# Performance work log

Hardware: AMD Instinct MI355X
Metric: run time of the kernel (lower is better)

The kernel has to match this reference:

```python
import jax, jax.numpy as jnp
import numpy as np

B, N, F, C = 8, 256, 59, 128
BOX = 20.0
EPS = 1e-5


def _bn(y, g, b, m, v):
    # eval-mode BatchNorm1d over the channel (last) axis
    return (y - m) * jax.lax.rsqrt(v + EPS) * g + b


def setup_inputs() -> dict:
    key = jax.random.key(0)
    ks = jax.random.split(key, 12)
    x = jax.random.normal(ks[0], (B, N, F), jnp.float32)
    pos = jax.random.uniform(ks[1], (B, N, 3), jnp.float32) * BOX
    nrm = jax.random.normal(ks[2], (B, N, 3), jnp.float32)
    normal = nrm / jnp.linalg.norm(nrm, axis=-1, keepdims=True)
    s_in = 1.0 / np.sqrt(F)
    W_lin = jax.random.normal(ks[3], (C, F), jnp.float32) * s_in
    W_src = jax.random.normal(ks[4], (C, F), jnp.float32) * s_in
    W_dst = jax.random.normal(ks[5], (C, F), jnp.float32) * s_in
    pos_w = jax.random.normal(ks[6], (C, 6), jnp.float32) * (1.0 / np.sqrt(6.0))
    pos_b = jax.random.normal(ks[7], (C,), jnp.float32) * 0.02
    attn_w = jax.random.normal(ks[8], (C, C), jnp.float32) * (1.0 / np.sqrt(C))
    attn_b = jax.random.normal(ks[9], (C,), jnp.float32) * 0.02
    pos_bn_g = 1.0 + 0.1 * jax.random.normal(ks[10], (C,), jnp.float32)
    attn_bn_g = 1.0 + 0.1 * jax.random.normal(ks[11], (C,), jnp.float32)
    zeros = jnp.zeros((C,), jnp.float32)
    ones = jnp.ones((C,), jnp.float32)
    return {
        'x': x, 'pos': pos, 'normal': normal,
        'W_lin': W_lin, 'W_src': W_src, 'W_dst': W_dst,
        'pos_w': pos_w, 'pos_b': pos_b,
        'pos_bn_g': pos_bn_g, 'pos_bn_b': zeros, 'pos_bn_m': zeros, 'pos_bn_v': ones,
        'attn_w': attn_w, 'attn_b': attn_b,
        'attn_bn_g': attn_bn_g, 'attn_bn_b': zeros, 'attn_bn_m': zeros, 'attn_bn_v': ones,
        'r': 5,
    }


def reference(x, pos, normal, W_lin, W_src, W_dst, pos_w, pos_b,
              pos_bn_g, pos_bn_b, pos_bn_m, pos_bn_v,
              attn_w, attn_b, attn_bn_g, attn_bn_b, attn_bn_m, attn_bn_v, r):
    r = jnp.float32(r)
    # linear projections (bias-free, as in PyG PointTransformerConv)
    v = jnp.einsum('bnf,cf->bnc', x, W_lin)      # values
    a_src = jnp.einsum('bnf,cf->bnc', x, W_src)  # alpha for source j
    a_dst = jnp.einsum('bnf,cf->bnc', x, W_dst)  # alpha for dest   i
    # relative geometry, axis 1 = receiver i, axis 2 = sender j
    rel_pos = pos[:, :, None, :] - pos[:, None, :, :]          # [B,i,j,3]
    rel_nrm = normal[:, :, None, :] - normal[:, None, :, :]    # [B,i,j,3]
    relf = jnp.concatenate([rel_pos, rel_nrm], axis=-1)        # [B,i,j,6]
    # pos_nn = Linear(6,C) + BN + ReLU (eval)
    delta = jax.nn.relu(_bn(jnp.einsum('bijk,ck->bijc', relf, pos_w) + pos_b,
                            pos_bn_g, pos_bn_b, pos_bn_m, pos_bn_v))
    # attn_nn(alpha_i - alpha_j + delta)
    alpha_arg = a_dst[:, :, None, :] - a_src[:, None, :, :] + delta
    scores = jax.nn.relu(_bn(jnp.einsum('bijc,dc->bijd', alpha_arg, attn_w) + attn_b,
                             attn_bn_g, attn_bn_b, attn_bn_m, attn_bn_v))
    # radius mask within each graph (self-loops included, dist 0 <= r)
    dist2 = jnp.sum(rel_pos * rel_pos, axis=-1)                # [B,i,j]
    mask = (dist2 <= r * r)[..., None]                         # [B,i,j,1]
    attn = jax.nn.softmax(jnp.where(mask, scores, -jnp.inf), axis=2)
    # per-channel vector attention over neighbors j: sum_j attn * (v_j + delta)
    out = jnp.sum(attn * (v[:, None, :, :] + delta), axis=2)   # [B,i,C]
    return out
```

## Files before the change

kernel.cpp:

```cpp
#include <hip/hip_runtime.h>

typedef _Float16 h2 __attribute__((ext_vector_type(2)));
typedef _Float16 f16x8 __attribute__((ext_vector_type(8)));
typedef float f32x4 __attribute__((ext_vector_type(4)));
typedef unsigned int uint32;

#define BB 8
#define NN 256
#define FF 59
#define CC 128
#define EPSV 1e-5f

#define WS_V     0
#define WS_ASRC  (WS_V + BB*NN*CC)
#define WS_ADST  (WS_ASRC + BB*NN*CC)
#define WS_PWT   (WS_ADST + BB*NN*CC)
#define WS_T1    (WS_PWT + 6*CC)
#define WS_T2    (WS_T1 + CC)
#define WS_WTB   (WS_T2 + CC)

__global__ __launch_bounds__(256) void prep_kernel(
    const float* __restrict__ x, const float* __restrict__ W_lin,
    const float* __restrict__ W_src, const float* __restrict__ W_dst,
    const float* __restrict__ pos_w, const float* __restrict__ pos_b,
    const float* __restrict__ pos_g, const float* __restrict__ pos_bb,
    const float* __restrict__ pos_m, const float* __restrict__ pos_v,
    const float* __restrict__ attn_w, const float* __restrict__ attn_b,
    const float* __restrict__ attn_g, const float* __restrict__ attn_bb,
    const float* __restrict__ attn_m, const float* __restrict__ attn_v,
    float* __restrict__ ws)
{
    int blk = blockIdx.x;
    int tid = threadIdx.x;
    if (blk < 768) {
        int type = blk >> 8;
        int g    = blk & 255;
        int b    = g >> 5;
        int n0   = (g & 31) * 8;
        const float* W = (type == 0) ? W_lin : (type == 1) ? W_src : W_dst;
        float* outp = ws + ((type == 0) ? WS_V : (type == 1) ? WS_ASRC : WS_ADST);
        __shared__ float Wl[CC * FF];
        __shared__ float xs[8 * 60];
        for (int idx = tid; idx < CC * FF; idx += 256) Wl[idx] = W[idx];
        const float* xrow = x + (size_t)(b * NN + n0) * FF;
        for (int idx = tid; idx < 8 * 60; idx += 256) {
            int r = idx / 60, f = idx - r * 60;
            xs[idx] = (f < FF) ? xrow[r * FF + f] : 0.f;
        }
        __syncthreads();
        int c = tid & 127, h = tid >> 7;
        const float* wrow = &Wl[c * FF];
        float acc[4];
#pragma unroll
        for (int q = 0; q < 4; ++q) acc[q] = 0.f;
#pragma unroll 2
        for (int f4 = 0; f4 < 14; ++f4) {
            float w0 = wrow[f4 * 4 + 0];
            float w1 = wrow[f4 * 4 + 1];
            float w2 = wrow[f4 * 4 + 2];
            float w3 = wrow[f4 * 4 + 3];
#pragma unroll
            for (int q = 0; q < 4; ++q) {
                float4 xq = *(const float4*)&xs[(h * 4 + q) * 60 + f4 * 4];
                acc[q] = fmaf(w0, xq.x, acc[q]);
                acc[q] = fmaf(w1, xq.y, acc[q]);
                acc[q] = fmaf(w2, xq.z, acc[q]);
                acc[q] = fmaf(w3, xq.w, acc[q]);
            }
        }
        {
            float w0 = wrow[56], w1 = wrow[57], w2 = wrow[58];
#pragma unroll
            for (int q = 0; q < 4; ++q) {
                const float* xr = &xs[(h * 4 + q) * 60];
                acc[q] = fmaf(w0, xr[56], acc[q]);
                acc[q] = fmaf(w1, xr[57], acc[q]);
                acc[q] = fmaf(w2, xr[58], acc[q]);
            }
        }
#pragma unroll
        for (int q = 0; q < 4; ++q) {
            int n = n0 + h * 4 + q;
            outp[(b * NN + n) * CC + c] = acc[q];
        }
    } else {
        __shared__ float S2s[CC];
        if (tid < CC) {
            int c = tid;
            float S1 = rsqrtf(pos_v[c] + EPSV) * pos_g[c];
            ws[WS_T1 + c] = (pos_b[c] - pos_m[c]) * S1 + pos_bb[c];
#pragma unroll
            for (int k = 0; k < 6; ++k) ws[WS_PWT + k * CC + c] = pos_w[c * 6 + k] * S1;
            float S2 = rsqrtf(attn_v[c] + EPSV) * attn_g[c];
            S2s[c] = S2;
            ws[WS_T2 + c] = (attn_b[c] - attn_m[c]) * S2 + attn_bb[c];
        }
        __syncthreads();
        uint4* wtbp = (uint4*)(ws + WS_WTB);
        for (int idx = tid; idx < 32 * 64; idx += 256) {
            int l = idx & 63, ts = idx >> 6;
            int t = ts >> 2, s = ts & 3;
            int d  = t * 16 + (l & 15);
            int c0 = s * 32 + ((l >> 4) << 3);
            float S2 = S2s[d];
            float4 w0 = *(const float4*)&attn_w[d * CC + c0];
            float4 w1 = *(const float4*)&attn_w[d * CC + c0 + 4];
            h2 p0, p1, p2, p3;
            p0.x = (_Float16)(w0.x * S2); p0.y = (_Float16)(w0.y * S2);
            p1.x = (_Float16)(w0.z * S2); p1.y = (_Float16)(w0.w * S2);
            p2.x = (_Float16)(w1.x * S2); p2.y = (_Float16)(w1.y * S2);
            p3.x = (_Float16)(w1.z * S2); p3.y = (_Float16)(w1.w * S2);
            uint4 o;
            o.x = __builtin_bit_cast(uint32, p0);
            o.y = __builtin_bit_cast(uint32, p1);
            o.z = __builtin_bit_cast(uint32, p2);
            o.w = __builtin_bit_cast(uint32, p3);
            wtbp[idx] = o;
        }
    }
}

__global__ __launch_bounds__(256, 4) void main_kernel(
    const float* __restrict__ pos, const float* __restrict__ nrm,
    const int* __restrict__ rptr, const float* __restrict__ ws,
    float* __restrict__ out)
{
    const float* v    = ws + WS_V;
    const float* asrc = ws + WS_ASRC;
    const float* adst = ws + WS_ADST;
    const float* pwt  = ws + WS_PWT;
    const float* T1   = ws + WS_T1;
    const float* T2   = ws + WS_T2;

    int blk = blockIdx.x;
    int b  = blk >> 7;
    int i0 = (blk & 127) * 2;
    int tid = threadIdx.x;

    __shared__ float relf[NN * 6];
    __shared__ int   jlist[NN];
    __shared__ int   wcnt[4];
    __shared__ int   cnt_s;
    __shared__ _Float16 alpha_h[16 * 136];
    __shared__ float    u_lds[16 * 132];

    int c    = tid & 127;
    int half = tid >> 7;
    int w    = tid >> 6;
    int lane = tid & 63;

    f16x8 bf[2][4];
    {
        const uint4* wtb = (const uint4*)(ws + WS_WTB);
#pragma unroll
        for (int tt = 0; tt < 2; ++tt)
#pragma unroll
            for (int s = 0; s < 4; ++s)
                bf[tt][s] = __builtin_bit_cast(f16x8,
                    wtb[((w * 2 + tt) * 4 + s) * 64 + lane]);
    }
    float T2a = T2[w * 32 + (lane & 15)];
    float T2b = T2[w * 32 + 16 + (lane & 15)];
    float pw[6];
#pragma unroll
    for (int k = 0; k < 6; ++k) pw[k] = pwt[k * CC + c];
    float T1c = T1[c];
    int rv = rptr[0];
    float r2 = (float)(rv * rv);

    for (int ii = 0; ii < 2; ++ii) {
        int i = i0 + ii;
        float adst_c = adst[(b * NN + i) * CC + c];
        const float* pib = pos + (size_t)(b * NN + i) * 3;
        const float* nib = nrm + (size_t)(b * NN + i) * 3;
        float pix = pib[0], piy = pib[1], piz = pib[2];
        float nix = nib[0], niy = nib[1], niz = nib[2];
        {
            int j = tid;
            const float* pj = pos + (size_t)(b * NN + j) * 3;
            const float* nj = nrm + (size_t)(b * NN + j) * 3;
            float dx = pix - pj[0], dy = piy - pj[1], dz = piz - pj[2];
            float ex = nix - nj[0], ey = niy - nj[1], ez = niz - nj[2];
            float d2 = dx * dx + dy * dy + dz * dz;
            bool valid = (d2 <= r2);
            unsigned long long m = __ballot(valid);
            if (lane == 0) wcnt[w] = __popcll(m);
            __syncthreads();
            int off = 0;
            for (int w2 = 0; w2 < w; ++w2) off += wcnt[w2];
            if (tid == 0) cnt_s = wcnt[0] + wcnt[1] + wcnt[2] + wcnt[3];
            int rank = __popcll(m & ((1ull << lane) - 1ull));
            if (valid) {
                int s = off + rank;
                jlist[s] = j;
                relf[s * 6 + 0] = dx; relf[s * 6 + 1] = dy; relf[s * 6 + 2] = dz;
                relf[s * 6 + 3] = ex; relf[s * 6 + 4] = ey; relf[s * 6 + 5] = ez;
            }
        }
        __syncthreads();
        int cnt = cnt_s;

        float pse0 = 0.f, pov0 = 0.f, pse1 = 0.f, pov1 = 0.f;

        for (int base = 0; base < cnt; base += 16) {
            if (base) __syncthreads();
            int tcnt = min(16, cnt - base);
#pragma unroll
            for (int q = 0; q < 8; ++q) {
                int s = 2 * q + half;
                if (s < tcnt) {
                    int js = base + s;
                    int j  = jlist[js];
                    const float2* rp = (const float2*)&relf[js * 6];
                    float2 r0 = rp[0], r1 = rp[1], r2f = rp[2];
                    float dsum = T1c;
                    dsum = fmaf(pw[0], r0.x, dsum);
                    dsum = fmaf(pw[1], r0.y, dsum);
                    dsum = fmaf(pw[2], r1.x, dsum);
                    dsum = fmaf(pw[3], r1.y, dsum);
                    dsum = fmaf(pw[4], r2f.x, dsum);
                    dsum = fmaf(pw[5], r2f.y, dsum);
                    float delta = fmaxf(dsum, 0.f);
                    alpha_h[s * 136 + c] = (_Float16)(adst_c - asrc[(b * NN + j) * CC + c] + delta);
                    u_lds[s * 132 + c]   = v[(b * NN + j) * CC + c] + delta;
                }
            }
            __syncthreads();
            f32x4 acc0 = {T2a, T2a, T2a, T2a};
            f32x4 acc1 = {T2b, T2b, T2b, T2b};
            {
                const _Float16* arow = &alpha_h[(lane & 15) * 136 + ((lane >> 4) << 3)];
#pragma unroll
                for (int s = 0; s < 4; ++s) {
                    f16x8 af = *(const f16x8*)(arow + s * 32);
                    acc0 = __builtin_amdgcn_mfma_f32_16x16x32_f16(af, bf[0][s], acc0, 0, 0, 0);
                    acc1 = __builtin_amdgcn_mfma_f32_16x16x32_f16(af, bf[1][s], acc1, 0, 0, 0);
                }
            }
            {
                int d0 = w * 32 + (lane & 15);
#pragma unroll
                for (int rg = 0; rg < 4; ++rg) {
                    int j = ((lane >> 4) << 2) + rg;
                    if (j < tcnt) {
                        float e0 = __expf(fmaxf(acc0[rg], 0.f));
                        float e1 = __expf(fmaxf(acc1[rg], 0.f));
                        pse0 += e0;
                        pov0 += e0 * u_lds[j * 132 + d0];
                        pse1 += e1;
                        pov1 += e1 * u_lds[j * 132 + d0 + 16];
                    }
                }
            }
        }

        pse0 += __shfl_xor(pse0, 16); pse0 += __shfl_xor(pse0, 32);
        pov0 += __shfl_xor(pov0, 16); pov0 += __shfl_xor(pov0, 32);
        pse1 += __shfl_xor(pse1, 16); pse1 += __shfl_xor(pse1, 32);
        pov1 += __shfl_xor(pov1, 16); pov1 += __shfl_xor(pov1, 32);
        if (lane < 16) {
            size_t o = (size_t)(b * NN + i) * CC + w * 32 + lane;
            out[o]      = pov0 / pse0;
            out[o + 16] = pov1 / pse1;
        }
    }
}

extern "C" void kernel_launch(void* const* d_in, const int* in_sizes, int n_in,
                              void* d_out, int out_size, void* d_ws, size_t ws_size,
                              hipStream_t stream) {
    const float* x      = (const float*)d_in[0];
    const float* pos    = (const float*)d_in[1];
    const float* normal = (const float*)d_in[2];
    const float* W_lin  = (const float*)d_in[3];
    const float* W_src  = (const float*)d_in[4];
    const float* W_dst  = (const float*)d_in[5];
    const float* pos_w  = (const float*)d_in[6];
    const float* pos_b  = (const float*)d_in[7];
    const float* pos_g  = (const float*)d_in[8];
    const float* pos_bb = (const float*)d_in[9];
    const float* pos_m  = (const float*)d_in[10];
    const float* pos_v  = (const float*)d_in[11];
    const float* attn_w = (const float*)d_in[12];
    const float* attn_b = (const float*)d_in[13];
    const float* attn_g = (const float*)d_in[14];
    const float* attn_bb= (const float*)d_in[15];
    const float* attn_m = (const float*)d_in[16];
    const float* attn_v = (const float*)d_in[17];
    const int*   rptr   = (const int*)d_in[18];
    float* ws  = (float*)d_ws;
    float* out = (float*)d_out;

    prep_kernel<<<dim3(769), dim3(256), 0, stream>>>(
        x, W_lin, W_src, W_dst, pos_w, pos_b, pos_g, pos_bb, pos_m, pos_v,
        attn_w, attn_b, attn_g, attn_bb, attn_m, attn_v, ws);
    main_kernel<<<dim3(1024), dim3(256), 0, stream>>>(pos, normal, rptr, ws, out);
}
```

Baseline: 109.9 us.

## Interleave asrc/v, pad pos+normal, and build both neighbor lists upfront

The prep kernel now writes a_src and v interleaved as float2 pairs, and packs pos and normal into padded 8-float records. The main kernel builds the neighbor lists for both receivers in a single pass with one barrier, instead of a separate compaction per receiver. It loads both a_dst values at the start and fetches a_src and v with one 8-byte load per neighbor. Shared buffers are duplicated per receiver and the u_lds stride changes from 132 to 130, which raises LDS use and may change bank conflicts and occupancy.

```diff
diff --git a/kernel.cpp b/kernel.cpp
--- a/kernel.cpp
+++ b/kernel.cpp
@@ -11,16 +11,18 @@
 #define CC 128
 #define EPSV 1e-5f
 
-#define WS_V     0
-#define WS_ASRC  (WS_V + BB*NN*CC)
-#define WS_ADST  (WS_ASRC + BB*NN*CC)
+#define WS_AV    0
+#define WS_ADST  (WS_AV + 2*BB*NN*CC)
 #define WS_PWT   (WS_ADST + BB*NN*CC)
 #define WS_T1    (WS_PWT + 6*CC)
 #define WS_T2    (WS_T1 + CC)
 #define WS_WTB   (WS_T2 + CC)
+#define WS_POSN  (WS_WTB + 8192)
 
 __global__ __launch_bounds__(256) void prep_kernel(
-    const float* __restrict__ x, const float* __restrict__ W_lin,
+    const float* __restrict__ x, const float* __restrict__ pos,
+    const float* __restrict__ nrm,
+    const float* __restrict__ W_lin,
     const float* __restrict__ W_src, const float* __restrict__ W_dst,
     const float* __restrict__ pos_w, const float* __restrict__ pos_b,
     const float* __restrict__ pos_g, const float* __restrict__ pos_bb,
@@ -38,7 +40,6 @@
         int b    = g >> 5;
         int n0   = (g & 31) * 8;
         const float* W = (type == 0) ? W_lin : (type == 1) ? W_src : W_dst;
-        float* outp = ws + ((type == 0) ? WS_V : (type == 1) ? WS_ASRC : WS_ADST);
         __shared__ float Wl[CC * FF];
         __shared__ float xs[8 * 60];
         for (int idx = tid; idx < CC * FF; idx += 256) Wl[idx] = W[idx];
@@ -78,10 +79,21 @@
                 acc[q] = fmaf(w2, xr[58], acc[q]);
             }
         }
-#pragma unroll
-        for (int q = 0; q < 4; ++q) {
-            int n = n0 + h * 4 + q;
-            outp[(b * NN + n) * CC + c] = acc[q];
+        if (type == 2) {
+            float* outp = ws + WS_ADST;
+#pragma unroll
+            for (int q = 0; q < 4; ++q) {
+                int n = n0 + h * 4 + q;
+                outp[(b * NN + n) * CC + c] = acc[q];
+            }
+        } else {
+            float* avp = ws + WS_AV;
+            int sub = (type == 0) ? 1 : 0;
+#pragma unroll
+            for (int q = 0; q < 4; ++q) {
+                int n = n0 + h * 4 + q;
+                avp[((size_t)(b * NN + n) * CC + c) * 2 + sub] = acc[q];
+            }
         }
     } else {
         __shared__ float S2s[CC];
@@ -94,6 +106,17 @@
             float S2 = rsqrtf(attn_v[c] + EPSV) * attn_g[c];
             S2s[c] = S2;
             ws[WS_T2 + c] = (attn_b[c] - attn_m[c]) * S2 + attn_bb[c];
+        }
+        for (int idx = tid; idx < BB * NN; idx += 256) {
+            float* dst = ws + WS_POSN + (size_t)idx * 8;
+            dst[0] = pos[idx * 3 + 0];
+            dst[1] = pos[idx * 3 + 1];
+            dst[2] = pos[idx * 3 + 2];
+            dst[3] = nrm[idx * 3 + 0];
+            dst[4] = nrm[idx * 3 + 1];
+            dst[5] = nrm[idx * 3 + 2];
+            dst[6] = 0.f;
+            dst[7] = 0.f;
         }
         __syncthreads();
         uint4* wtbp = (uint4*)(ws + WS_WTB);
@@ -121,12 +144,10 @@
 }
 
 __global__ __launch_bounds__(256, 4) void main_kernel(
-    const float* __restrict__ pos, const float* __restrict__ nrm,
     const int* __restrict__ rptr, const float* __restrict__ ws,
     float* __restrict__ out)
 {
-    const float* v    = ws + WS_V;
-    const float* asrc = ws + WS_ASRC;
+    const float2* av  = (const float2*)(ws + WS_AV);
     const float* adst = ws + WS_ADST;
     const float* pwt  = ws + WS_PWT;
     const float* T1   = ws + WS_T1;
@@ -137,12 +158,11 @@
     int i0 = (blk & 127) * 2;
     int tid = threadIdx.x;
 
-    __shared__ float relf[NN * 6];
-    __shared__ int   jlist[NN];
-    __shared__ int   wcnt[4];
-    __shared__ int   cnt_s;
-    __shared__ _Float16 alpha_h[16 * 136];
-    __shared__ float    u_lds[16 * 132];
+    __shared__ __align__(16) float relf[2][NN * 6];
+    __shared__ int jlist[2][NN];
+    __shared__ int wcnt[2][4];
+    __shared__ __align__(16) _Float16 alpha_h[2][16 * 136];
+    __shared__ float u_lds[2][16 * 130];
 
     int c    = tid & 127;
     int half = tid >> 7;
@@ -165,41 +185,55 @@
 #pragma unroll
     for (int k = 0; k < 6; ++k) pw[k] = pwt[k * CC + c];
     float T1c = T1[c];
+    float adc0 = adst[(size_t)(b * NN + i0) * CC + c];
+    float adc1 = adst[(size_t)(b * NN + i0 + 1) * CC + c];
     int rv = rptr[0];
     float r2 = (float)(rv * rv);
 
+    int cnt0, cnt1;
+    {
+        int j = tid;
+        const float4* pj = (const float4*)(ws + WS_POSN + (size_t)(b * NN + j) * 8);
+        float4 ja = pj[0], jb = pj[1];
+        const float4* pi0 = (const float4*)(ws + WS_POSN + (size_t)(b * NN + i0) * 8);
+        const float4* pi1 = (const float4*)(ws + WS_POSN + (size_t)(b * NN + i0 + 1) * 8);
+        float4 ia0 = pi0[0], ib0 = pi0[1];
+        float4 ia1 = pi1[0], ib1 = pi1[1];
+        float dx0 = ia0.x - ja.x, dy0 = ia0.y - ja.y, dz0 = ia0.z - ja.z;
+        float ex0 = ia0.w - ja.w, ey0 = ib0.x - jb.x, ez0 = ib0.y - jb.y;
+        float dx1 = ia1.x - ja.x, dy1 = ia1.y - ja.y, dz1 = ia1.z - ja.z;
+        float ex1 = ia1.w - ja.w, ey1 = ib1.x - jb.x, ez1 = ib1.y - jb.y;
+        bool v0 = (dx0 * dx0 + dy0 * dy0 + dz0 * dz0) <= r2;
+        bool v1 = (dx1 * dx1 + dy1 * dy1 + dz1 * dz1) <= r2;
+        unsigned long long m0 = __ballot(v0);
+        unsigned long long m1 = __ballot(v1);
+        if (lane == 0) { wcnt[0][w] = __popcll(m0); wcnt[1][w] = __popcll(m1); }
+        __syncthreads();
+        int off0 = 0, off1 = 0;
+        for (int w2 = 0; w2 < w; ++w2) { off0 += wcnt[0][w2]; off1 += wcnt[1][w2]; }
+        unsigned long long lm = (1ull << lane) - 1ull;
+        if (v0) {
+            int s = off0 + __popcll(m0 & lm);
+            jlist[0][s] = j;
+            relf[0][s * 6 + 0] = dx0; relf[0][s * 6 + 1] = dy0; relf[0][s * 6 + 2] = dz0;
+            relf[0][s * 6 + 3] = ex0; relf[0][s * 6 + 4] = ey0; relf[0][s * 6 + 5] = ez0;
+        }
+        if (v1) {
+            int s = off1 + __popcll(m1 & lm);
+            jlist[1][s] = j;
+            relf[1][s * 6 + 0] = dx1; relf[1][s * 6 + 1] = dy1; relf[1][s * 6 + 2] = dz1;
+            relf[1][s * 6 + 3] = ex1; relf[1][s * 6 + 4] = ey1; relf[1][s * 6 + 5] = ez1;
+        }
+        cnt0 = wcnt[0][0] + wcnt[0][1] + wcnt[0][2] + wcnt[0][3];
+        cnt1 = wcnt[1][0] + wcnt[1][1] + wcnt[1][2] + wcnt[1][3];
+    }
+    __syncthreads();
+
+#pragma unroll
     for (int ii = 0; ii < 2; ++ii) {
         int i = i0 + ii;
-        float adst_c = adst[(b * NN + i) * CC + c];
-        const float* pib = pos + (size_t)(b * NN + i) * 3;
-        const float* nib = nrm + (size_t)(b * NN + i) * 3;
-        float pix = pib[0], piy = pib[1], piz = pib[2];
-        float nix = nib[0], niy = nib[1], niz = nib[2];
-        {
-            int j = tid;
-            const float* pj = pos + (size_t)(b * NN + j) * 3;
-            const float* nj = nrm + (size_t)(b * NN + j) * 3;
-            float dx = pix - pj[0], dy = piy - pj[1], dz = piz - pj[2];
-            float ex = nix - nj[0], ey = niy - nj[1], ez = niz - nj[2];
-            float d2 = dx * dx + dy * dy + dz * dz;
-            bool valid = (d2 <= r2);
-            unsigned long long m = __ballot(valid);
-            if (lane == 0) wcnt[w] = __popcll(m);
-            __syncthreads();
-            int off = 0;
-            for (int w2 = 0; w2 < w; ++w2) off += wcnt[w2];
-            if (tid == 0) cnt_s = wcnt[0] + wcnt[1] + wcnt[2] + wcnt[3];
-            int rank = __popcll(m & ((1ull << lane) - 1ull));
-            if (valid) {
-                int s = off + rank;
-                jlist[s] = j;
-                relf[s * 6 + 0] = dx; relf[s * 6 + 1] = dy; relf[s * 6 + 2] = dz;
-                relf[s * 6 + 3] = ex; relf[s * 6 + 4] = ey; relf[s * 6 + 5] = ez;
-            }
-        }
-        __syncthreads();
-        int cnt = cnt_s;
-
+        int cnt = ii ? cnt1 : cnt0;
+        float adc = ii ? adc1 : adc0;
         float pse0 = 0.f, pov0 = 0.f, pse1 = 0.f, pov1 = 0.f;
 
         for (int base = 0; base < cnt; base += 16) {
@@ -210,8 +244,8 @@
                 int s = 2 * q + half;
                 if (s < tcnt) {
                     int js = base + s;
-                    int j  = jlist[js];
-                    const float2* rp = (const float2*)&relf[js * 6];
+                    int j  = jlist[ii][js];
+                    const float2* rp = (const float2*)&relf[ii][js * 6];
                     float2 r0 = rp[0], r1 = rp[1], r2f = rp[2];
                     float dsum = T1c;
                     dsum = fmaf(pw[0], r0.x, dsum);
@@ -221,15 +255,16 @@
                     dsum = fmaf(pw[4], r2f.x, dsum);
                     dsum = fmaf(pw[5], r2f.y, dsum);
                     float delta = fmaxf(dsum, 0.f);
-                    alpha_h[s * 136 + c] = (_Float16)(adst_c - asrc[(b * NN + j) * CC + c] + delta);
-                    u_lds[s * 132 + c]   = v[(b * NN + j) * CC + c] + delta;
+                    float2 avj = av[(size_t)(b * NN + j) * CC + c];
+                    alpha_h[ii][s * 136 + c] = (_Float16)(adc - avj.x + delta);
+                    u_lds[ii][s * 130 + c]   = avj.y + delta;
                 }
             }
             __syncthreads();
             f32x4 acc0 = {T2a, T2a, T2a, T2a};
             f32x4 acc1 = {T2b, T2b, T2b, T2b};
             {
-                const _Float16* arow = &alpha_h[(lane & 15) * 136 + ((lane >> 4) << 3)];
+                const _Float16* arow = &alpha_h[ii][(lane & 15) * 136 + ((lane >> 4) << 3)];
 #pragma unroll
                 for (int s = 0; s < 4; ++s) {
                     f16x8 af = *(const f16x8*)(arow + s * 32);
@@ -246,9 +281,9 @@
                         float e0 = __expf(fmaxf(acc0[rg], 0.f));
                         float e1 = __expf(fmaxf(acc1[rg], 0.f));
                         pse0 += e0;
-                        pov0 += e0 * u_lds[j * 132 + d0];
+                        pov0 += e0 * u_lds[ii][j * 130 + d0];
                         pse1 += e1;
-                        pov1 += e1 * u_lds[j * 132 + d0 + 16];
+                        pov1 += e1 * u_lds[ii][j * 130 + d0 + 16];
                     }
                 }
             }
@@ -292,7 +327,7 @@
     float* out = (float*)d_out;
 
     prep_kernel<<<dim3(769), dim3(256), 0, stream>>>(
-        x, W_lin, W_src, W_dst, pos_w, pos_b, pos_g, pos_bb, pos_m, pos_v,
+        x, pos, normal, W_lin, W_src, W_dst, pos_w, pos_b, pos_g, pos_bb, pos_m, pos_v,
         attn_w, attn_b, attn_g, attn_bb, attn_m, attn_v, ws);
-    main_kernel<<<dim3(1024), dim3(256), 0, stream>>>(pos, normal, rptr, ws, out);
+    main_kernel<<<dim3(1024), dim3(256), 0, stream>>>(rptr, ws, out);
 }
```

After: 110.8 us. About the same (+0.8%).
